# Performance work log

Measured on AMD Instinct MI355X. Metric: run time of the kernel, lower is better.

Reference implementation:

```python
import jax, jax.numpy as jnp
import numpy as np

N_QUBITS = 8
N_LAYERS = 2


def _apply_1q(state, U, wire, n):
    # state: (bs, 2**n); U: (2,2) fixed or (bs,2,2) batched; wire 0 = most significant
    bs = state.shape[0]
    left = 2 ** wire
    right = 2 ** (n - wire - 1)
    s = state.reshape(bs, left, 2, right)
    if U.ndim == 2:
        s = jnp.einsum('ij,bljr->blir', U, s)
    else:
        s = jnp.einsum('bij,bljr->blir', U, s)
    return s.reshape(bs, -1)


def _apply_ctrl(state, U, control, target, n):
    # apply 2x2 U on `target` where `control` qubit is |1>
    bs = state.shape[0]
    left = 2 ** control
    right = 2 ** (n - control - 1)
    s = state.reshape(bs, left, 2, right)
    s0 = s[:, :, 0, :].reshape(bs, -1)
    s1 = s[:, :, 1, :].reshape(bs, -1)
    t = target if target < control else target - 1  # target index among remaining n-1 wires
    s1 = _apply_1q(s1, U, t, n - 1)
    s = jnp.stack([s0.reshape(bs, left, right), s1.reshape(bs, left, right)], axis=2)
    return s.reshape(bs, -1)


def _rz_batched(theta):
    h = 0.5 * theta
    c, s = jnp.cos(h), jnp.sin(h)
    z = jnp.zeros_like(c)
    row0 = jnp.stack([c - 1j * s, z + 0j], axis=-1)
    row1 = jnp.stack([z + 0j, c + 1j * s], axis=-1)
    return jnp.stack([row0, row1], axis=-2).astype(jnp.complex64)  # (bs,2,2)


def _ry_batched(theta):
    h = 0.5 * theta
    c, s = jnp.cos(h), jnp.sin(h)
    row0 = jnp.stack([c, -s], axis=-1)
    row1 = jnp.stack([s, c], axis=-1)
    return jnp.stack([row0, row1], axis=-2).astype(jnp.complex64)


def _rx_fixed(theta):
    h = 0.5 * theta
    c, s = jnp.cos(h), jnp.sin(h)
    return jnp.stack([jnp.stack([c + 0j, -1j * s]), jnp.stack([-1j * s, c + 0j])]).astype(jnp.complex64)


def _ry_fixed(theta):
    h = 0.5 * theta
    c, s = jnp.cos(h), jnp.sin(h)
    return jnp.stack([jnp.stack([c + 0j, -s + 0j]), jnp.stack([s + 0j, c + 0j])]).astype(jnp.complex64)


def _circuit(X, weights):
    bs, L = X.shape
    n = N_QUBITS
    vpq = L // n + 1  # var_per_qubit
    state = jnp.zeros((bs, 2 ** n), jnp.complex64).at[:, 0].set(1.0)
    H = jnp.asarray(np.array([[1, 1], [1, -1]], np.complex64) / np.sqrt(2))
    # encoding: Hadamard then alternating RZ/RY per qubit
    for q in range(n):
        state = _apply_1q(state, H, q, n)
        for i in range(vpq):
            idx = q * vpq + i
            if idx >= L:
                break
            th = X[:, idx]
            U = _rz_batched(th) if i % 2 == 0 else _ry_batched(th)
            state = _apply_1q(state, U, q, n)
    # entangling ring: layer 0 -> CRX, layer 1 -> CRY ((l+1)%2==0 -> CRY)
    for l in range(N_LAYERS):
        for i in range(n):
            th = weights[l, i]
            U = _ry_fixed(th) if (l + 1) % 2 == 0 else _rx_fixed(th)
            state = _apply_ctrl(state, U, i, (i + 1) % n, n)
    # PauliZ expectation on each wire
    p = state.real ** 2 + state.imag ** 2  # (bs, 256)
    outs = []
    for q in range(n):
        pq = p.reshape(bs, 2 ** q, 2, -1).sum(axis=(1, 3))  # (bs, 2)
        outs.append(pq[:, 0] - pq[:, 1])
    return jnp.stack(outs, axis=1)  # (bs, 8)


def setup_inputs() -> dict:
    key = jax.random.key(0)
    k1, k2 = jax.random.split(key)
    X = jax.random.normal(k1, (16384, 64), dtype=jnp.float32)
    weights = jax.random.normal(k2, (N_LAYERS, N_LAYERS * N_QUBITS), dtype=jnp.float32)
    return {"X": X, "weights": weights}


def reference(X, weights):
    return _circuit(X, weights)
```

## Files before the change

kernel.cpp:

```cpp
#include <hip/hip_runtime.h>

#define DEV __device__ __forceinline__
typedef float f32x2 __attribute__((ext_vector_type(2)));
typedef float f32x4 __attribute__((ext_vector_type(4)));

DEV float shflx(float v, int m) { return __shfl_xor(v, m, 64); }
DEV float rdlane(float v, int l) {
  return __int_as_float(__builtin_amdgcn_readlane(__float_as_int(v), l));
}
DEV f32x2 pkfma(f32x2 a, f32x2 b, f32x2 c) { return __builtin_elementwise_fma(a, b, c); }
DEV f32x2 splat(float x) { return (f32x2){x, x}; }
DEV f32x2 swap2(f32x2 v) { return __builtin_shufflevector(v, v, 1, 0); }
DEV f32x2 cmul(f32x2 P, f32x2 F) {
  f32x2 t = swap2(P);
  f32x2 m = {-t.x, t.y};
  return pkfma(splat(F.y), m, splat(F.x) * P);
}

__global__ __launch_bounds__(256) void qsim_kernel(const float* __restrict__ X,
                                                   const float* __restrict__ W,
                                                   float* __restrict__ out, int bs) {
  const int lane = threadIdx.x & 63;
  const int wave = blockIdx.x * (blockDim.x >> 6) + (threadIdx.x >> 6);
  const int b0 = wave * 4;
  if (b0 >= bs) return;
  const int nElem = (bs - b0) < 4 ? (bs - b0) : 4;

  float w = W[(((lane & 15) >> 3) << 4) + (lane & 7)];
  float sw, cw;
  __sincosf(0.5f * w, &sw, &cw);

  const int ce = (lane >> 3) & 3;
  const int cq = lane & 7;
  int bb = b0 + ce; bb = bb >= bs ? bs - 1 : bb;
  const float* Xrow = X + (size_t)bb * 64;
  float ang[9];
#pragma unroll
  for (int i = 0; i < 9; ++i) {
    int idx = cq * 9 + i;
    idx = idx > 63 ? 63 : idx;
    ang[i] = Xrow[idx];
  }
  const float Hc = 0.70710678118654752440f;
  f32x2 A = {Hc, 0.f}, B = {Hc, 0.f};
#pragma unroll
  for (int i = 0; i < 9; ++i) {
    float s, c;
    __sincosf(0.5f * ang[i], &s, &c);
    if (i > 0) {
      bool dead = (cq == 7);
      c = dead ? 1.f : c;
      s = dead ? 0.f : s;
    }
    if ((i & 1) == 0) {
      f32x2 nA = pkfma((f32x2){s, -s}, swap2(A), splat(c) * A);
      f32x2 nB = pkfma((f32x2){-s, s}, swap2(B), splat(c) * B);
      A = nA; B = nB;
    } else {
      f32x2 nA = pkfma(splat(-s), B, splat(c) * A);
      f32x2 nB = pkfma(splat(c), B, splat(s) * A);
      A = nA; B = nB;
    }
  }

  __shared__ f32x4 ldsAB[4][32];
  const int wvid = (threadIdx.x >> 6) & 3;
  if (lane < 32) ldsAB[wvid][lane] = (f32x4){A.x, A.y, B.x, B.y};
  __builtin_amdgcn_wave_barrier();

  const f32x2* base = (const f32x2*)&ldsAB[wvid][0];
  f32x2 amp[4][4];
#pragma unroll
  for (int e = 0; e < 4; ++e) {
    int bit0 = (lane >> 5) & 1;
    f32x2 P = base[(e * 8 + 0) * 2 + bit0];
#pragma unroll
    for (int q = 1; q <= 5; ++q) {
      int bit = (lane >> (5 - q)) & 1;
      P = cmul(P, base[(e * 8 + q) * 2 + bit]);
    }
    f32x4 F6 = ldsAB[wvid][e * 8 + 6];
    f32x4 F7 = ldsAB[wvid][e * 8 + 7];
    f32x2 A6 = {F6.x, F6.y}, B6 = {F6.z, F6.w};
    f32x2 A7 = {F7.x, F7.y}, B7 = {F7.z, F7.w};
    f32x2 t0 = cmul(P, A6), t1 = cmul(P, B6);
    amp[e][0] = cmul(t0, A7);
    amp[e][1] = cmul(t0, B7);
    amp[e][2] = cmul(t1, A7);
    amp[e][3] = cmul(t1, B7);
  }

#pragma unroll
  for (int l = 0; l < 2; ++l) {
    const bool isCRX = (l == 0);
#pragma unroll
    for (int i = 0; i < 8; ++i) {
      const float cg = rdlane(cw, l * 8 + i);
      const float sg = rdlane(sw, l * 8 + i);
      if (i <= 4) {
        const int d = 1 << (4 - i);
        const bool act = (lane >> (5 - i)) & 1;
        const float c1 = act ? cg : 1.f;
        const float s1 = act ? sg : 0.f;
        const f32x2 C2 = splat(c1);
        if (isCRX) {
          const f32x2 S2 = {s1, -s1};
#pragma unroll
          for (int e = 0; e < 4; ++e)
#pragma unroll
            for (int r = 0; r < 4; ++r) {
              f32x2 p;
              p.x = shflx(amp[e][r].y, d);
              p.y = shflx(amp[e][r].x, d);
              amp[e][r] = pkfma(S2, p, C2 * amp[e][r]);
            }
        } else {
          const bool side = (lane >> (4 - i)) & 1;
          const float sp = side ? s1 : -s1;
          const f32x2 SP = splat(sp);
#pragma unroll
          for (int e = 0; e < 4; ++e)
#pragma unroll
            for (int r = 0; r < 4; ++r) {
              f32x2 p;
              p.x = shflx(amp[e][r].x, d);
              p.y = shflx(amp[e][r].y, d);
              amp[e][r] = pkfma(SP, p, C2 * amp[e][r]);
            }
        }
      } else if (i == 5) {
        const bool act = lane & 1;
        const float c1 = act ? cg : 1.f;
        const float s1 = act ? sg : 0.f;
        const f32x2 C2 = splat(c1);
#pragma unroll
        for (int e = 0; e < 4; ++e) {
          f32x2 A0 = amp[e][0], A1 = amp[e][1], A2 = amp[e][2], A3 = amp[e][3];
          if (isCRX) {
            const f32x2 S2 = {s1, -s1};
            amp[e][0] = pkfma(S2, swap2(A2), C2 * A0);
            amp[e][2] = pkfma(S2, swap2(A0), C2 * A2);
            amp[e][1] = pkfma(S2, swap2(A3), C2 * A1);
            amp[e][3] = pkfma(S2, swap2(A1), C2 * A3);
          } else {
            const f32x2 SN = splat(-s1), SPp = splat(s1);
            amp[e][0] = pkfma(SN, A2, C2 * A0);
            amp[e][2] = pkfma(SPp, A0, C2 * A2);
            amp[e][1] = pkfma(SN, A3, C2 * A1);
            amp[e][3] = pkfma(SPp, A1, C2 * A3);
          }
        }
      } else if (i == 6) {
        const f32x2 C2 = splat(cg);
#pragma unroll
        for (int e = 0; e < 4; ++e) {
          f32x2 A2 = amp[e][2], A3 = amp[e][3];
          if (isCRX) {
            const f32x2 S2 = {sg, -sg};
            amp[e][2] = pkfma(S2, swap2(A3), C2 * A2);
            amp[e][3] = pkfma(S2, swap2(A2), C2 * A3);
          } else {
            amp[e][2] = pkfma(splat(-sg), A3, C2 * A2);
            amp[e][3] = pkfma(splat(sg), A2, C2 * A3);
          }
        }
      } else {
        const f32x2 C2 = splat(cg);
        if (isCRX) {
          const f32x2 S2 = {sg, -sg};
#pragma unroll
          for (int e = 0; e < 4; ++e)
#pragma unroll
            for (int r = 1; r < 4; r += 2) {
              f32x2 p;
              p.x = shflx(amp[e][r].y, 32);
              p.y = shflx(amp[e][r].x, 32);
              amp[e][r] = pkfma(S2, p, C2 * amp[e][r]);
            }
        } else {
          const bool side = (lane >> 5) & 1;
          const float sp = side ? sg : -sg;
          const f32x2 SP = splat(sp);
#pragma unroll
          for (int e = 0; e < 4; ++e)
#pragma unroll
            for (int r = 1; r < 4; r += 2) {
              f32x2 p;
              p.x = shflx(amp[e][r].x, 32);
              p.y = shflx(amp[e][r].y, 32);
              amp[e][r] = pkfma(SP, p, C2 * amp[e][r]);
            }
        }
      }
    }
  }

  float whtv[4], d6s[4], d7s[4];
#pragma unroll
  for (int e = 0; e < 4; ++e) {
    float p0 = fmaf(amp[e][0].x, amp[e][0].x, amp[e][0].y * amp[e][0].y);
    float p1 = fmaf(amp[e][1].x, amp[e][1].x, amp[e][1].y * amp[e][1].y);
    float p2 = fmaf(amp[e][2].x, amp[e][2].x, amp[e][2].y * amp[e][2].y);
    float p3 = fmaf(amp[e][3].x, amp[e][3].x, amp[e][3].y * amp[e][3].y);
    float t01 = p0 + p1, t23 = p2 + p3;
    float s4 = t01 + t23;
    float d6 = t01 - t23;
    float d7 = (p0 + p2) - (p1 + p3);
    float wv_ = s4;
#pragma unroll
    for (int k = 0; k < 6; ++k) {
      float pp = shflx(wv_, 1 << k);
      float neg = ((lane >> k) & 1) ? -wv_ : wv_;
      wv_ = pp + neg;
    }
#pragma unroll
    for (int d = 1; d < 64; d <<= 1) { d6 += shflx(d6, d); d7 += shflx(d7, d); }
    whtv[e] = wv_; d6s[e] = d6; d7s[e] = d7;
  }

  const int qs = lane & 7;
  const int eid = lane >> 3;
  const int src = 32 >> qs;
  float outv = 0.f;
#pragma unroll
  for (int e = 0; e < 4; ++e) {
    float g = __shfl(whtv[e], src, 64);
    float v = (qs == 6) ? d6s[e] : (qs == 7) ? d7s[e] : g;
    outv = (eid == e) ? v : outv;
  }
  if (eid < nElem) out[(size_t)b0 * 8 + lane] = outv;
}

extern "C" void kernel_launch(void* const* d_in, const int* in_sizes, int n_in,
                              void* d_out, int out_size, void* d_ws, size_t ws_size,
                              hipStream_t stream) {
  const float* X = (const float*)d_in[0];
  const float* W = (const float*)d_in[1];
  float* out = (float*)d_out;
  int bs = in_sizes[0] / 64;
  int waves = (bs + 3) / 4;
  const int waves_per_block = 4;
  const int threads = waves_per_block * 64;
  int blocks = (waves + waves_per_block - 1) / waves_per_block;
  hipLaunchKernelGGL(qsim_kernel, dim3(blocks), dim3(threads), 0, stream, X, W, out, bs);
}
```

Baseline: 75.76 us.

## Halve batch elements per wave and use DPP lane swaps for small shuffles

Each wave now simulates two batch elements instead of four, which doubles the wave count and reduces per-thread register state. Cross-lane exchanges for xor distances 1, 2 and 8 use DPP moves instead of ds_bpermute shuffles. The reduction merges the two parity sums into a packed vector, and launch bounds request higher occupancy. The cost is duplicated per-wave setup work (weight sincos, angle loads), spread over fewer elements per wave.

```diff
diff --git a/kernel.cpp b/kernel.cpp
--- a/kernel.cpp
+++ b/kernel.cpp
@@ -17,20 +17,61 @@
   return pkfma(splat(F.y), m, splat(F.x) * P);
 }
 
-__global__ __launch_bounds__(256) void qsim_kernel(const float* __restrict__ X,
-                                                   const float* __restrict__ W,
-                                                   float* __restrict__ out, int bs) {
+template <int CTRL>
+DEV float dppmov(float v) {
+  return __int_as_float(__builtin_amdgcn_update_dpp(
+      0, __float_as_int(v), CTRL, 0xf, 0xf, true));
+}
+template <int M>
+DEV float xorl(float v) {
+  if constexpr (M == 1)      return dppmov<0xB1>(v);
+  else if constexpr (M == 2) return dppmov<0x4E>(v);
+  else if constexpr (M == 8) return dppmov<0x128>(v);
+  else                       return shflx(v, M);
+}
+
+template <int D, bool CRX, int R0, int RS>
+DEV void gate_x(f32x2 amp[2][4], int lane, float c1, float s1) {
+  const f32x2 C2 = splat(c1);
+  if constexpr (CRX) {
+    const f32x2 S2 = {s1, -s1};
+#pragma unroll
+    for (int e = 0; e < 2; ++e)
+#pragma unroll
+      for (int r = R0; r < 4; r += RS) {
+        f32x2 p;
+        p.x = xorl<D>(amp[e][r].y);
+        p.y = xorl<D>(amp[e][r].x);
+        amp[e][r] = pkfma(S2, p, C2 * amp[e][r]);
+      }
+  } else {
+    const float sp = (lane & D) ? s1 : -s1;
+    const f32x2 SP = splat(sp);
+#pragma unroll
+    for (int e = 0; e < 2; ++e)
+#pragma unroll
+      for (int r = R0; r < 4; r += RS) {
+        f32x2 p;
+        p.x = xorl<D>(amp[e][r].x);
+        p.y = xorl<D>(amp[e][r].y);
+        amp[e][r] = pkfma(SP, p, C2 * amp[e][r]);
+      }
+  }
+}
+
+__global__ __launch_bounds__(256, 8) void qsim_kernel(const float* __restrict__ X,
+                                                      const float* __restrict__ W,
+                                                      float* __restrict__ out, int bs) {
   const int lane = threadIdx.x & 63;
   const int wave = blockIdx.x * (blockDim.x >> 6) + (threadIdx.x >> 6);
-  const int b0 = wave * 4;
+  const int b0 = wave * 2;
   if (b0 >= bs) return;
-  const int nElem = (bs - b0) < 4 ? (bs - b0) : 4;
 
   float w = W[(((lane & 15) >> 3) << 4) + (lane & 7)];
   float sw, cw;
   __sincosf(0.5f * w, &sw, &cw);
 
-  const int ce = (lane >> 3) & 3;
+  const int ce = (lane >> 3) & 1;
   const int cq = lane & 7;
   int bb = b0 + ce; bb = bb >= bs ? bs - 1 : bb;
   const float* Xrow = X + (size_t)bb * 64;
@@ -63,15 +104,15 @@
     }
   }
 
-  __shared__ f32x4 ldsAB[4][32];
+  __shared__ f32x4 ldsAB[4][16];
   const int wvid = (threadIdx.x >> 6) & 3;
-  if (lane < 32) ldsAB[wvid][lane] = (f32x4){A.x, A.y, B.x, B.y};
+  if (lane < 16) ldsAB[wvid][lane] = (f32x4){A.x, A.y, B.x, B.y};
   __builtin_amdgcn_wave_barrier();
 
   const f32x2* base = (const f32x2*)&ldsAB[wvid][0];
-  f32x2 amp[4][4];
-#pragma unroll
-  for (int e = 0; e < 4; ++e) {
+  f32x2 amp[2][4];
+#pragma unroll
+  for (int e = 0; e < 2; ++e) {
     int bit0 = (lane >> 5) & 1;
     f32x2 P = base[(e * 8 + 0) * 2 + bit0];
 #pragma unroll
@@ -90,145 +131,102 @@
     amp[e][3] = cmul(t1, B7);
   }
 
+#define LANE_GATE(G, CBIT, D)                                         \
+  {                                                                   \
+    const float cg = rdlane(cw, G), sg = rdlane(sw, G);               \
+    const bool act = (lane >> (CBIT)) & 1;                            \
+    const float c1 = act ? cg : 1.f, s1 = act ? sg : 0.f;             \
+    if (isCRX) gate_x<D, true, 0, 1>(amp, lane, c1, s1);              \
+    else       gate_x<D, false, 0, 1>(amp, lane, c1, s1);             \
+  }
 #pragma unroll
   for (int l = 0; l < 2; ++l) {
     const bool isCRX = (l == 0);
-#pragma unroll
-    for (int i = 0; i < 8; ++i) {
-      const float cg = rdlane(cw, l * 8 + i);
-      const float sg = rdlane(sw, l * 8 + i);
-      if (i <= 4) {
-        const int d = 1 << (4 - i);
-        const bool act = (lane >> (5 - i)) & 1;
-        const float c1 = act ? cg : 1.f;
-        const float s1 = act ? sg : 0.f;
-        const f32x2 C2 = splat(c1);
+    LANE_GATE(l * 8 + 0, 5, 16)
+    LANE_GATE(l * 8 + 1, 4, 8)
+    LANE_GATE(l * 8 + 2, 3, 4)
+    LANE_GATE(l * 8 + 3, 2, 2)
+    LANE_GATE(l * 8 + 4, 1, 1)
+    {
+      const float cg = rdlane(cw, l * 8 + 5), sg = rdlane(sw, l * 8 + 5);
+      const bool act = lane & 1;
+      const float c1 = act ? cg : 1.f, s1 = act ? sg : 0.f;
+      const f32x2 C2 = splat(c1);
+#pragma unroll
+      for (int e = 0; e < 2; ++e) {
+        f32x2 A0 = amp[e][0], A1 = amp[e][1], A2 = amp[e][2], A3 = amp[e][3];
         if (isCRX) {
           const f32x2 S2 = {s1, -s1};
-#pragma unroll
-          for (int e = 0; e < 4; ++e)
-#pragma unroll
-            for (int r = 0; r < 4; ++r) {
-              f32x2 p;
-              p.x = shflx(amp[e][r].y, d);
-              p.y = shflx(amp[e][r].x, d);
-              amp[e][r] = pkfma(S2, p, C2 * amp[e][r]);
-            }
+          amp[e][0] = pkfma(S2, swap2(A2), C2 * A0);
+          amp[e][2] = pkfma(S2, swap2(A0), C2 * A2);
+          amp[e][1] = pkfma(S2, swap2(A3), C2 * A1);
+          amp[e][3] = pkfma(S2, swap2(A1), C2 * A3);
         } else {
-          const bool side = (lane >> (4 - i)) & 1;
-          const float sp = side ? s1 : -s1;
-          const f32x2 SP = splat(sp);
-#pragma unroll
-          for (int e = 0; e < 4; ++e)
-#pragma unroll
-            for (int r = 0; r < 4; ++r) {
-              f32x2 p;
-              p.x = shflx(amp[e][r].x, d);
-              p.y = shflx(amp[e][r].y, d);
-              amp[e][r] = pkfma(SP, p, C2 * amp[e][r]);
-            }
+          amp[e][0] = pkfma(splat(-s1), A2, C2 * A0);
+          amp[e][2] = pkfma(splat(s1), A0, C2 * A2);
+          amp[e][1] = pkfma(splat(-s1), A3, C2 * A1);
+          amp[e][3] = pkfma(splat(s1), A1, C2 * A3);
         }
-      } else if (i == 5) {
-        const bool act = lane & 1;
-        const float c1 = act ? cg : 1.f;
-        const float s1 = act ? sg : 0.f;
-        const f32x2 C2 = splat(c1);
-#pragma unroll
-        for (int e = 0; e < 4; ++e) {
-          f32x2 A0 = amp[e][0], A1 = amp[e][1], A2 = amp[e][2], A3 = amp[e][3];
-          if (isCRX) {
-            const f32x2 S2 = {s1, -s1};
-            amp[e][0] = pkfma(S2, swap2(A2), C2 * A0);
-            amp[e][2] = pkfma(S2, swap2(A0), C2 * A2);
-            amp[e][1] = pkfma(S2, swap2(A3), C2 * A1);
-            amp[e][3] = pkfma(S2, swap2(A1), C2 * A3);
-          } else {
-            const f32x2 SN = splat(-s1), SPp = splat(s1);
-            amp[e][0] = pkfma(SN, A2, C2 * A0);
-            amp[e][2] = pkfma(SPp, A0, C2 * A2);
-            amp[e][1] = pkfma(SN, A3, C2 * A1);
-            amp[e][3] = pkfma(SPp, A1, C2 * A3);
-          }
-        }
-      } else if (i == 6) {
-        const f32x2 C2 = splat(cg);
-#pragma unroll
-        for (int e = 0; e < 4; ++e) {
-          f32x2 A2 = amp[e][2], A3 = amp[e][3];
-          if (isCRX) {
-            const f32x2 S2 = {sg, -sg};
-            amp[e][2] = pkfma(S2, swap2(A3), C2 * A2);
-            amp[e][3] = pkfma(S2, swap2(A2), C2 * A3);
-          } else {
-            amp[e][2] = pkfma(splat(-sg), A3, C2 * A2);
-            amp[e][3] = pkfma(splat(sg), A2, C2 * A3);
-          }
-        }
-      } else {
-        const f32x2 C2 = splat(cg);
+      }
+    }
+    {
+      const float cg = rdlane(cw, l * 8 + 6), sg = rdlane(sw, l * 8 + 6);
+      const f32x2 C2 = splat(cg);
+#pragma unroll
+      for (int e = 0; e < 2; ++e) {
+        f32x2 A2 = amp[e][2], A3 = amp[e][3];
         if (isCRX) {
           const f32x2 S2 = {sg, -sg};
-#pragma unroll
-          for (int e = 0; e < 4; ++e)
-#pragma unroll
-            for (int r = 1; r < 4; r += 2) {
-              f32x2 p;
-              p.x = shflx(amp[e][r].y, 32);
-              p.y = shflx(amp[e][r].x, 32);
-              amp[e][r] = pkfma(S2, p, C2 * amp[e][r]);
-            }
+          amp[e][2] = pkfma(S2, swap2(A3), C2 * A2);
+          amp[e][3] = pkfma(S2, swap2(A2), C2 * A3);
         } else {
-          const bool side = (lane >> 5) & 1;
-          const float sp = side ? sg : -sg;
-          const f32x2 SP = splat(sp);
-#pragma unroll
-          for (int e = 0; e < 4; ++e)
-#pragma unroll
-            for (int r = 1; r < 4; r += 2) {
-              f32x2 p;
-              p.x = shflx(amp[e][r].x, 32);
-              p.y = shflx(amp[e][r].y, 32);
-              amp[e][r] = pkfma(SP, p, C2 * amp[e][r]);
-            }
+          amp[e][2] = pkfma(splat(-sg), A3, C2 * A2);
+          amp[e][3] = pkfma(splat(sg), A2, C2 * A3);
         }
       }
     }
-  }
-
-  float whtv[4], d6s[4], d7s[4];
-#pragma unroll
-  for (int e = 0; e < 4; ++e) {
+    {
+      const float cg = rdlane(cw, l * 8 + 7), sg = rdlane(sw, l * 8 + 7);
+      if (isCRX) gate_x<32, true, 1, 2>(amp, lane, cg, sg);
+      else       gate_x<32, false, 1, 2>(amp, lane, cg, sg);
+    }
+  }
+#undef LANE_GATE
+
+  float whtv[2], d6s[2], d7s[2];
+#pragma unroll
+  for (int e = 0; e < 2; ++e) {
     float p0 = fmaf(amp[e][0].x, amp[e][0].x, amp[e][0].y * amp[e][0].y);
     float p1 = fmaf(amp[e][1].x, amp[e][1].x, amp[e][1].y * amp[e][1].y);
     float p2 = fmaf(amp[e][2].x, amp[e][2].x, amp[e][2].y * amp[e][2].y);
     float p3 = fmaf(amp[e][3].x, amp[e][3].x, amp[e][3].y * amp[e][3].y);
     float t01 = p0 + p1, t23 = p2 + p3;
-    float s4 = t01 + t23;
-    float d6 = t01 - t23;
-    float d7 = (p0 + p2) - (p1 + p3);
-    float wv_ = s4;
-#pragma unroll
-    for (int k = 0; k < 6; ++k) {
-      float pp = shflx(wv_, 1 << k);
-      float neg = ((lane >> k) & 1) ? -wv_ : wv_;
-      wv_ = pp + neg;
-    }
-#pragma unroll
-    for (int d = 1; d < 64; d <<= 1) { d6 += shflx(d6, d); d7 += shflx(d7, d); }
-    whtv[e] = wv_; d6s[e] = d6; d7s[e] = d7;
+    float wv = t01 + t23;
+    f32x2 D = {t01 - t23,
+               (p0 + p2) - (p1 + p3)};
+#define STAGE(K, M)                                         \
+    {                                                       \
+      float pp = xorl<M>(wv);                               \
+      wv = pp + (((lane >> K) & 1) ? -wv : wv);             \
+      f32x2 pd;                                             \
+      pd.x = xorl<M>(D.x);                                  \
+      pd.y = xorl<M>(D.y);                                  \
+      D = D + pd;                                           \
+    }
+    STAGE(0, 1) STAGE(1, 2) STAGE(2, 4) STAGE(3, 8) STAGE(4, 16) STAGE(5, 32)
+#undef STAGE
+    whtv[e] = wv; d6s[e] = D.x; d7s[e] = D.y;
   }
 
   const int qs = lane & 7;
-  const int eid = lane >> 3;
+  const int eid = (lane >> 3) & 1;
   const int src = 32 >> qs;
-  float outv = 0.f;
-#pragma unroll
-  for (int e = 0; e < 4; ++e) {
-    float g = __shfl(whtv[e], src, 64);
-    float v = (qs == 6) ? d6s[e] : (qs == 7) ? d7s[e] : g;
-    outv = (eid == e) ? v : outv;
-  }
-  if (eid < nElem) out[(size_t)b0 * 8 + lane] = outv;
+  float g0 = __shfl(whtv[0], src, 64);
+  float g1 = __shfl(whtv[1], src, 64);
+  float v0 = (qs == 6) ? d6s[0] : (qs == 7) ? d7s[0] : g0;
+  float v1 = (qs == 6) ? d6s[1] : (qs == 7) ? d7s[1] : g1;
+  float val = eid ? v1 : v0;
+  if (lane < 16 && (b0 + eid) < bs) out[(size_t)b0 * 8 + lane] = val;
 }
 
 extern "C" void kernel_launch(void* const* d_in, const int* in_sizes, int n_in,
@@ -238,7 +236,7 @@
   const float* W = (const float*)d_in[1];
   float* out = (float*)d_out;
   int bs = in_sizes[0] / 64;
-  int waves = (bs + 3) / 4;
+  int waves = (bs + 1) / 2;
   const int waves_per_block = 4;
   const int threads = waves_per_block * 64;
   int blocks = (waves + waves_per_block - 1) / waves_per_block;
```

Result: faster. 67.08 us (-11.5%).
